# Kernel tuning notes

Measured on AMD Instinct MI355X. Metric: run time of the kernel, lower is better.

Reference implementation:

```python
import math
import jax, jax.numpy as jnp
import numpy as np

B, S, G, D = 16, 256, 2048, 512
H = 8
DK = D // H  # per-head key dim
E = 8        # num experts
TOPK = 2


def setup_inputs() -> dict:
    key = jax.random.key(0)
    ks = jax.random.split(key, 12)
    init = lambda k, shape, fan_in: jax.random.uniform(k, shape, jnp.float32, -1.0, 1.0) / np.sqrt(fan_in)
    return {
        'query': jax.random.normal(ks[0], (B, S, D), jnp.float32),
        'key': jax.random.normal(ks[1], (B, G, D), jnp.float32),
        'value': jax.random.normal(ks[2], (B, G, D), jnp.float32),  # unused by module (MHA uses h=key)
        'logit_key': jax.random.normal(ks[3], (B, G, D), jnp.float32),
        'attn_mask': jnp.zeros((B, G), dtype=bool),
        'Wq': init(ks[4], (H, D, DK), D),
        'Wk': init(ks[5], (H, D, DK), D),
        'Wv': init(ks[6], (H, D, DK), D),
        'Wo': init(ks[7], (H, DK, D), DK),
        'w_gate': jnp.zeros((D, E), jnp.float32) + init(ks[8], (D, E), D) * 0.0 + init(ks[9], (D, E), D),
        'expert_w': init(ks[10], (E, D, D), D),
    }


def _mha_glimpse(query, h, attn_mask, Wq, Wk, Wv, Wo):
    # Kool-style MHA: K and V both derived from h
    Q = jnp.einsum('bsd,hdk->bhsk', query, Wq)
    K = jnp.einsum('bgd,hdk->bhgk', h, Wk)
    V = jnp.einsum('bgd,hdk->bhgk', h, Wv)
    scores = jnp.einsum('bhsk,bhgk->bhsg', Q, K) / math.sqrt(DK)
    # 2D mask (B,G) expanded over heads and steps; True = masked out
    mask = attn_mask[:, None, None, :]
    scores = jnp.where(mask, jnp.float32(-1e9), scores)
    attn = jax.nn.softmax(scores, axis=-1)
    heads = jnp.einsum('bhsg,bhgk->bhsk', attn, V)
    return jnp.einsum('bhsk,hkd->bsd', heads, Wo)


def _moe(x, w_gate, expert_w):
    # x: (N, D). Noisy top-k gating, eval mode (no noise): clean logits -> top-k -> softmax over top-k.
    logits = x @ w_gate                                  # (N, E)
    top_vals, top_idx = jax.lax.top_k(logits, TOPK)      # (N, k)
    top_gates = jax.nn.softmax(top_vals, axis=-1)        # (N, k)
    gates = jnp.sum(jax.nn.one_hot(top_idx, E, dtype=x.dtype) * top_gates[..., None], axis=1)  # (N, E)
    expert_out = jnp.einsum('nd,edo->neo', x, expert_w)  # dense combine: same math as dispatch/scatter
    return jnp.einsum('ne,neo->no', gates, expert_out)


def reference(query, key, value, logit_key, attn_mask, Wq, Wk, Wv, Wo, w_gate, expert_w):
    glimpse = _mha_glimpse(query, key, attn_mask, Wq, Wk, Wv, Wo)  # (B, S, D)
    gm = _moe(glimpse.reshape(B * S, D), w_gate, expert_w).reshape(B, S, D)
    logits = jnp.einsum('bsd,bgd->bsg', gm, logit_key) / math.sqrt(D)
    return logits
```

## Files before the change

kernel.cpp:

```cpp
#include <hip/hip_runtime.h>

#define B_  16
#define S_  256
#define G_  2048
#define D_  512
#define H_  8
#define DK_ 64
#define E_  8

typedef _Float16 half8  __attribute__((ext_vector_type(8)));
typedef _Float16 half4v __attribute__((ext_vector_type(4)));
typedef float    floatx4 __attribute__((ext_vector_type(4)));

#define GLDS(g, l) __builtin_amdgcn_global_load_lds( \
    (const __attribute__((address_space(1))) void*)(g), \
    (__attribute__((address_space(3))) void*)(l), 16, 0, 0)

__global__ void __launch_bounds__(256) split_f16(
    const float* __restrict__ src, _Float16* __restrict__ hi,
    _Float16* __restrict__ lo, int n4)
{
    int i = blockIdx.x * 256 + threadIdx.x;
    if (i >= n4) return;
    float4 v = ((const float4*)src)[i];
    half4v h, l;
    h[0] = (_Float16)v.x; h[1] = (_Float16)v.y;
    h[2] = (_Float16)v.z; h[3] = (_Float16)v.w;
    l[0] = (_Float16)(v.x - (float)h[0]); l[1] = (_Float16)(v.y - (float)h[1]);
    l[2] = (_Float16)(v.z - (float)h[2]); l[3] = (_Float16)(v.w - (float)h[3]);
    ((half4v*)hi)[i] = h;
    ((half4v*)lo)[i] = l;
}

__global__ void __launch_bounds__(256) transpose_split(
    const float* __restrict__ src, _Float16* __restrict__ hi,
    _Float16* __restrict__ lo, int R, int C)
{
    __shared__ float T[32][33];
    const int tid = threadIdx.x;
    const long zo = (long)blockIdx.z * R * C;
    const int r0 = blockIdx.y * 32, c0 = blockIdx.x * 32;
#pragma unroll
    for (int p = 0; p < 4; ++p) {
        int i = tid + p * 256;
        int lr = i >> 5, lc = i & 31;
        T[lr][lc] = src[zo + (long)(r0 + lr) * C + (c0 + lc)];
    }
    __syncthreads();
#pragma unroll
    for (int p = 0; p < 4; ++p) {
        int i = tid + p * 256;
        int orr = i >> 5, oc = i & 31;
        float v = T[oc][orr];
        _Float16 h = (_Float16)v;
        long o = zo + (long)(c0 + orr) * R + (r0 + oc);
        hi[o] = h;
        lo[o] = (_Float16)(v - (float)h);
    }
}

__global__ void __launch_bounds__(256) gemm_f16x3(
    const _Float16* __restrict__ Ah, const _Float16* __restrict__ Al,
    const _Float16* __restrict__ Bh, const _Float16* __restrict__ Bl,
    float* __restrict__ C, _Float16* __restrict__ Chi, _Float16* __restrict__ Clo,
    long ldc, long sAz, long sBz, long sCz, float alpha)
{
    __shared__ _Float16 Ash[128 * 32], Asl[128 * 32];
    __shared__ _Float16 Bsh[128 * 32], Bsl[128 * 32];
    const int tid = threadIdx.x;
    const int w = tid >> 6, lane = tid & 63;
    const int quad = lane >> 4, tn = lane & 15;
    const int wm = (w >> 1) * 64, wn = (w & 1) * 64;
    const int z = blockIdx.z;
    const long m0 = (long)blockIdx.y * 128;
    const long n0 = (long)blockIdx.x * 128;
    const _Float16* Agh = Ah + (z * sAz + m0) * 512;
    const _Float16* Agl = Al + (z * sAz + m0) * 512;
    const _Float16* Bgh = Bh + (z * sBz + n0) * 512;
    const _Float16* Bgl = Bl + (z * sBz + n0) * 512;
    const long glane = (long)(lane >> 2) * 512 + (lane & 3) * 8;

    floatx4 acc[4][4] = {};

    for (int k0 = 0; k0 < 512; k0 += 32) {
#pragma unroll
        for (int cc = 0; cc < 2; ++cc) {
            const int c = 2 * w + cc;
            const long go = (long)c * 16 * 512 + glane + k0;
            GLDS(Agh + go, Ash + c * 512);
            GLDS(Agl + go, Asl + c * 512);
            GLDS(Bgh + go, Bsh + c * 512);
            GLDS(Bgl + go, Bsl + c * 512);
        }
        asm volatile("s_waitcnt vmcnt(0)" ::: "memory");
        __syncthreads();

        half8 ah[4], al[4], bh[4], bl[4];
#pragma unroll
        for (int t = 0; t < 4; ++t) {
            ah[t] = *(const half8*)&Ash[(wm + t * 16 + tn) * 32 + quad * 8];
            al[t] = *(const half8*)&Asl[(wm + t * 16 + tn) * 32 + quad * 8];
            bh[t] = *(const half8*)&Bsh[(wn + t * 16 + tn) * 32 + quad * 8];
            bl[t] = *(const half8*)&Bsl[(wn + t * 16 + tn) * 32 + quad * 8];
        }
#pragma unroll
        for (int i = 0; i < 4; ++i)
#pragma unroll
            for (int j = 0; j < 4; ++j) {
                acc[i][j] = __builtin_amdgcn_mfma_f32_16x16x32_f16(ah[i], bh[j], acc[i][j], 0, 0, 0);
                acc[i][j] = __builtin_amdgcn_mfma_f32_16x16x32_f16(ah[i], bl[j], acc[i][j], 0, 0, 0);
                acc[i][j] = __builtin_amdgcn_mfma_f32_16x16x32_f16(al[i], bh[j], acc[i][j], 0, 0, 0);
            }
        __syncthreads();
    }

#pragma unroll
    for (int i = 0; i < 4; ++i) {
        const long row0 = m0 + wm + i * 16 + quad * 4;
#pragma unroll
        for (int r = 0; r < 4; ++r) {
            const long row = row0 + r;
#pragma unroll
            for (int j = 0; j < 4; ++j) {
                float v = acc[i][j][r] * alpha;
                const long o = (long)z * sCz + row * ldc + n0 + wn + j * 16 + tn;
                if (C) C[o] = v;
                if (Chi) {
                    _Float16 hh = (_Float16)v;
                    Chi[o] = hh;
                    Clo[o] = (_Float16)(v - (float)hh);
                }
            }
        }
    }
}

__global__ void __launch_bounds__(512) flash_mfma(
    const _Float16* __restrict__ qh, const _Float16* __restrict__ qlo,
    const _Float16* __restrict__ kh, const _Float16* __restrict__ kl,
    const _Float16* __restrict__ vh, const _Float16* __restrict__ vl,
    const unsigned char* __restrict__ mask,
    _Float16* __restrict__ hd_hi, _Float16* __restrict__ hd_lo)
{
    __shared__ half8 KH[512], KL[512], VH[512], VL[512];
    __shared__ float PLb[8 * 16 * 64];
    const int tid = threadIdx.x;
    const int wid = tid >> 6, lane = tid & 63;
    const int quad = lane >> 4, tn = lane & 15;
    const int h = blockIdx.y, b = blockIdx.z;
    const int s_base = blockIdx.x * 128 + wid * 16;
    const long tok0 = (long)b * S_ + s_base;
    float* Pw = PLb + wid * (16 * 64);
    const unsigned char* mb = mask + (long)b * G_;

    const long qoff = (tok0 + tn) * 512 + h * 64 + quad * 8;
    half8 qfh[2], qfl[2];
    qfh[0] = *(const half8*)(qh + qoff);
    qfh[1] = *(const half8*)(qh + qoff + 32);
    qfl[0] = *(const half8*)(qlo + qoff);
    qfl[1] = *(const half8*)(qlo + qoff + 32);

    const int sr = tid >> 3, sg = tid & 7;
    const int swz = sr * 8 + (sg ^ (sr & 7));
    const long kgbase = (long)b * G_ * 512 + h * 64 + sg * 8;
    const long vgbase = (long)(h * 64 + sr) * (B_ * G_) + (long)b * G_ + sg * 8;

    half8 pk0 = *(const half8*)(kh + kgbase + (long)sr * 512);
    half8 pk1 = *(const half8*)(kl + kgbase + (long)sr * 512);
    half8 pk2 = *(const half8*)(vh + vgbase);
    half8 pk3 = *(const half8*)(vl + vgbase);

    floatx4 accO[4] = {};
    float lsum[4] = {0.f, 0.f, 0.f, 0.f};

    for (int t = 0; t < 32; ++t) {
        KH[swz] = pk0; KL[swz] = pk1; VH[swz] = pk2; VL[swz] = pk3;
        __syncthreads();
        if (t < 31) {
            const int g1 = (t + 1) * 64;
            pk0 = *(const half8*)(kh + kgbase + (long)(g1 + sr) * 512);
            pk1 = *(const half8*)(kl + kgbase + (long)(g1 + sr) * 512);
            pk2 = *(const half8*)(vh + vgbase + g1);
            pk3 = *(const half8*)(vl + vgbase + g1);
        }
        const int g0 = t * 64;

        floatx4 accS[4] = {};
#pragma unroll
        for (int k0 = 0; k0 < 2; ++k0)
#pragma unroll
            for (int nj = 0; nj < 4; ++nj) {
                const int row = nj * 16 + tn;
                const int gi = row * 8 + ((k0 * 4 + quad) ^ (row & 7));
                half8 kbh = KH[gi], kbl = KL[gi];
                accS[nj] = __builtin_amdgcn_mfma_f32_16x16x32_f16(qfh[k0], kbh, accS[nj], 0, 0, 0);
                accS[nj] = __builtin_amdgcn_mfma_f32_16x16x32_f16(qfh[k0], kbl, accS[nj], 0, 0, 0);
                accS[nj] = __builtin_amdgcn_mfma_f32_16x16x32_f16(qfl[k0], kbh, accS[nj], 0, 0, 0);
            }

        float rs[4] = {0.f, 0.f, 0.f, 0.f};
#pragma unroll
        for (int nj = 0; nj < 4; ++nj) {
            const bool mk = mb[g0 + nj * 16 + tn] != 0;
#pragma unroll
            for (int rr = 0; rr < 4; ++rr) {
                float p = __builtin_exp2f(accS[nj][rr]);
                p = mk ? 0.0f : p;
                accS[nj][rr] = p;
                rs[rr] += p;
            }
        }
#pragma unroll
        for (int rr = 0; rr < 4; ++rr) {
            float v = rs[rr];
            v += __shfl_xor(v, 1); v += __shfl_xor(v, 2);
            v += __shfl_xor(v, 4); v += __shfl_xor(v, 8);
            lsum[rr] += v;
        }

#pragma unroll
        for (int nj = 0; nj < 4; ++nj)
#pragma unroll
            for (int rr = 0; rr < 4; ++rr) {
                const int srow = quad * 4 + rr;
                const int c = nj * 16 + tn;
                Pw[srow * 64 + ((((c >> 2) ^ srow) & 15) << 2) + (c & 3)] = accS[nj][rr];
            }
        asm volatile("s_waitcnt lgkmcnt(0)" ::: "memory");

#pragma unroll
        for (int k0 = 0; k0 < 2; ++k0) {
            const int ga = k0 * 8 + quad * 2;
            floatx4 p0 = *(floatx4*)&Pw[tn * 64 + (((ga ^ tn) & 15) << 2)];
            floatx4 p1 = *(floatx4*)&Pw[tn * 64 + ((((ga + 1) ^ tn) & 15) << 2)];
            half8 ph, pl;
#pragma unroll
            for (int e = 0; e < 8; ++e) {
                const float x = (e < 4) ? p0[e & 3] : p1[e & 3];
                const float hi = __uint_as_float(__float_as_uint(x) & 0xFFFFE000u);
                ph[e] = (_Float16)hi;
                pl[e] = (_Float16)(x - hi);
            }
#pragma unroll
            for (int nj = 0; nj < 4; ++nj) {
                const int row = nj * 16 + tn;
                const int gi = row * 8 + ((k0 * 4 + quad) ^ (row & 7));
                half8 vbh = VH[gi], vbl = VL[gi];
                accO[nj] = __builtin_amdgcn_mfma_f32_16x16x32_f16(ph, vbh, accO[nj], 0, 0, 0);
                accO[nj] = __builtin_amdgcn_mfma_f32_16x16x32_f16(ph, vbl, accO[nj], 0, 0, 0);
                accO[nj] = __builtin_amdgcn_mfma_f32_16x16x32_f16(pl, vbh, accO[nj], 0, 0, 0);
            }
        }
        __syncthreads();
    }

#pragma unroll
    for (int rr = 0; rr < 4; ++rr) {
        const float inv = 1.0f / lsum[rr];
        const long rbase = (tok0 + quad * 4 + rr) * 512 + h * 64 + tn;
#pragma unroll
        for (int nj = 0; nj < 4; ++nj) {
            const float o = accO[nj][rr] * inv;
            const _Float16 oh = (_Float16)o;
            hd_hi[rbase + nj * 16] = oh;
            hd_lo[rbase + nj * 16] = (_Float16)(o - (float)oh);
        }
    }
}

__global__ void __launch_bounds__(256) gate_topk(
    const _Float16* __restrict__ Xh, const _Float16* __restrict__ Xl,
    const float* __restrict__ wg, float* __restrict__ gates)
{
    __shared__ float W[512][8];
    __shared__ float Xs[256][37];
    const int tid = threadIdx.x;
    const int n0 = blockIdx.x * 256;
#pragma unroll
    for (int p = 0; p < 16; ++p) ((float*)W)[tid + p * 256] = wg[tid + p * 256];

    float acc[8] = {};
    for (int dc = 0; dc < 512; dc += 32) {
        __syncthreads();
#pragma unroll
        for (int p = 0; p < 8; ++p) {
            int f = tid + p * 256;
            int row = f >> 3, c4 = f & 7;
            long o = (long)(n0 + row) * 512 + dc + 4 * c4;
            half4v hv = *(const half4v*)(Xh + o);
            half4v lv = *(const half4v*)(Xl + o);
#pragma unroll
            for (int i = 0; i < 4; ++i) Xs[row][4 * c4 + i] = (float)hv[i] + (float)lv[i];
        }
        __syncthreads();
        for (int d2 = 0; d2 < 32; ++d2) {
            float xv = Xs[tid][d2];
#pragma unroll
            for (int e = 0; e < 8; ++e) acc[e] += xv * W[dc + d2][e];
        }
    }
    float v1 = -3.0e38f; int i1 = 0;
#pragma unroll
    for (int e = 0; e < 8; ++e) if (acc[e] > v1) { v1 = acc[e]; i1 = e; }
    float v2 = -3.0e38f; int i2 = -1;
#pragma unroll
    for (int e = 0; e < 8; ++e) if (e != i1 && acc[e] > v2) { v2 = acc[e]; i2 = e; }
    float t = __expf(v2 - v1);
    float g1 = 1.0f / (1.0f + t);
    float g2 = t / (1.0f + t);
#pragma unroll
    for (int e = 0; e < 8; ++e)
        gates[(long)(n0 + tid) * 8 + e] = (e == i1) ? g1 : ((e == i2) ? g2 : 0.0f);
}

__global__ void __launch_bounds__(256) combine_moe(
    const float* __restrict__ eo, const float* __restrict__ gates,
    _Float16* __restrict__ gh, _Float16* __restrict__ gl)
{
    const int idx = blockIdx.x * 256 + threadIdx.x;
    const int n = idx >> 7;
    const int c = (idx & 127) * 4;
    float g[8];
#pragma unroll
    for (int e = 0; e < 8; ++e) g[e] = gates[(long)n * 8 + e];
    float ax = 0.f, ay = 0.f, az = 0.f, aw = 0.f;
#pragma unroll
    for (int e = 0; e < 8; ++e) {
        if (g[e] != 0.0f) {
            float4 v = *(const float4*)(eo + (long)e * 2097152 + (long)n * 512 + c);
            ax += g[e] * v.x; ay += g[e] * v.y; az += g[e] * v.z; aw += g[e] * v.w;
        }
    }
    half4v h, l;
    h[0] = (_Float16)ax; h[1] = (_Float16)ay; h[2] = (_Float16)az; h[3] = (_Float16)aw;
    l[0] = (_Float16)(ax - (float)h[0]); l[1] = (_Float16)(ay - (float)h[1]);
    l[2] = (_Float16)(az - (float)h[2]); l[3] = (_Float16)(aw - (float)h[3]);
    *(half4v*)(gh + (long)n * 512 + c) = h;
    *(half4v*)(gl + (long)n * 512 + c) = l;
}

extern "C" void kernel_launch(void* const* d_in, const int* in_sizes, int n_in,
                              void* d_out, int out_size, void* d_ws, size_t ws_size,
                              hipStream_t stream) {
    const float* query     = (const float*)d_in[0];
    const float* key       = (const float*)d_in[1];
    const float* logit_key = (const float*)d_in[3];
    const unsigned char* mask = (const unsigned char*)d_in[4];
    const float* Wq = (const float*)d_in[5];
    const float* Wk = (const float*)d_in[6];
    const float* Wv = (const float*)d_in[7];
    const float* Wo = (const float*)d_in[8];
    const float* wg = (const float*)d_in[9];
    const float* Ew = (const float*)d_in[10];
    float* out = (float*)d_out;

    const size_t MBy = 1048576;
    char* W = (char*)d_ws;
    _Float16* q_hi  = (_Float16*)(W + 0 * MBy);
    _Float16* q_lo  = (_Float16*)(W + 4 * MBy);
    _Float16* kp_hi = (_Float16*)(W + 8 * MBy);
    _Float16* kp_lo = (_Float16*)(W + 40 * MBy);
    _Float16* vt_hi = (_Float16*)(W + 72 * MBy);
    _Float16* vt_lo = (_Float16*)(W + 104 * MBy);
    _Float16* kin_hi = (_Float16*)(W + 136 * MBy);
    _Float16* kin_lo = (_Float16*)(W + 168 * MBy);
    float*    eo    = (float*)(W + 136 * MBy);
    _Float16* lk_hi = (_Float16*)(W + 136 * MBy);
    _Float16* lk_lo = (_Float16*)(W + 168 * MBy);
    _Float16* wq_hi = (_Float16*)(W + 204 * MBy);
    _Float16* wq_lo = (_Float16*)(W + 204 * MBy + 524288);
    _Float16* wk_hi = (_Float16*)(W + 205 * MBy);
    _Float16* wk_lo = (_Float16*)(W + 205 * MBy + 524288);
    _Float16* wv_hi = (_Float16*)(W + 206 * MBy);
    _Float16* wv_lo = (_Float16*)(W + 206 * MBy + 524288);
    _Float16* wo_hi = (_Float16*)(W + 207 * MBy);
    _Float16* wo_lo = (_Float16*)(W + 207 * MBy + 524288);
    _Float16* ew_hi = (_Float16*)(W + 208 * MBy);
    _Float16* ew_lo = (_Float16*)(W + 212 * MBy);
    _Float16* qi_hi = (_Float16*)(W + 216 * MBy);
    _Float16* qi_lo = (_Float16*)(W + 220 * MBy);
    _Float16* hd_hi = (_Float16*)(W + 216 * MBy);
    _Float16* hd_lo = (_Float16*)(W + 220 * MBy);
    _Float16* gl_hi = (_Float16*)(W + 224 * MBy);
    _Float16* gl_lo = (_Float16*)(W + 228 * MBy);
    _Float16* gm_hi = (_Float16*)(W + 232 * MBy);
    _Float16* gm_lo = (_Float16*)(W + 236 * MBy);
    float*    gates = (float*)(W + 240 * MBy);

    dim3 blk(256);

    split_f16<<<dim3(16384), blk, 0, stream>>>(key, kin_hi, kin_lo, 4194304);
    split_f16<<<dim3(2048), blk, 0, stream>>>(query, qi_hi, qi_lo, 524288);
    transpose_split<<<dim3(2, 16, 8), blk, 0, stream>>>(Wq, wq_hi, wq_lo, 512, 64);
    transpose_split<<<dim3(2, 16, 8), blk, 0, stream>>>(Wk, wk_hi, wk_lo, 512, 64);
    transpose_split<<<dim3(2, 16, 8), blk, 0, stream>>>(Wv, wv_hi, wv_lo, 512, 64);
    transpose_split<<<dim3(16, 16, 1), blk, 0, stream>>>(Wo, wo_hi, wo_lo, 512, 512);
    transpose_split<<<dim3(16, 16, 8), blk, 0, stream>>>(Ew, ew_hi, ew_lo, 512, 512);

    gemm_f16x3<<<dim3(4, 32, 1), blk, 0, stream>>>(
        qi_hi, qi_lo, wq_hi, wq_lo, nullptr, q_hi, q_lo, 512, 0, 0, 0,
        0.1803368801111204f);
    gemm_f16x3<<<dim3(4, 256, 1), blk, 0, stream>>>(
        kin_hi, kin_lo, wk_hi, wk_lo, nullptr, kp_hi, kp_lo, 512, 0, 0, 0, 1.0f);
    gemm_f16x3<<<dim3(256, 4, 1), blk, 0, stream>>>(
        wv_hi, wv_lo, kin_hi, kin_lo, nullptr, vt_hi, vt_lo, (long)B_ * G_,
        0, 0, 0, 1.0f);

    flash_mfma<<<dim3(2, H_, B_), dim3(512), 0, stream>>>(
        q_hi, q_lo, kp_hi, kp_lo, vt_hi, vt_lo, mask, hd_hi, hd_lo);

    gemm_f16x3<<<dim3(4, 32, 1), blk, 0, stream>>>(
        hd_hi, hd_lo, wo_hi, wo_lo, nullptr, gl_hi, gl_lo, 512, 0, 0, 0, 1.0f);

    gate_topk<<<dim3(16), blk, 0, stream>>>(gl_hi, gl_lo, wg, gates);

    gemm_f16x3<<<dim3(4, 32, 8), blk, 0, stream>>>(
        gl_hi, gl_lo, ew_hi, ew_lo, eo, nullptr, nullptr, 512, 0, 512, 2097152, 1.0f);

    combine_moe<<<dim3(2048), blk, 0, stream>>>(eo, gates, gm_hi, gm_lo);

    split_f16<<<dim3(16384), blk, 0, stream>>>(logit_key, lk_hi, lk_lo, 4194304);

    gemm_f16x3<<<dim3(16, 2, 16), blk, 0, stream>>>(
        gm_hi, gm_lo, lk_hi, lk_lo, out, nullptr, nullptr, 2048,
        256, 2048, 524288, 0.04419417382415922f);
}
```

Measured before the change: 609.9 us.

## Split flash attention over key sequence halves and merge partials in a combine kernel

The flash attention grid is split into two halves along the key dimension G, doubling the block count from 256 to 512. Each block writes its unnormalized output accumulator and row sums in fp32 to a scratch region that reuses the freed key-input buffer. A new combine kernel adds the two partials, normalizes, and writes the hi/lo fp16 pair. The intent is to fill more CUs and hide latency in the attention stage, at the cost of an extra kernel launch and fp32 round trips through global memory.

New measurement: 627.1 us. +2.8%, slower.

```diff
diff --git a/kernel.cpp b/kernel.cpp
--- a/kernel.cpp
+++ b/kernel.cpp
@@ -140,7 +140,7 @@
     const _Float16* __restrict__ kh, const _Float16* __restrict__ kl,
     const _Float16* __restrict__ vh, const _Float16* __restrict__ vl,
     const unsigned char* __restrict__ mask,
-    _Float16* __restrict__ hd_hi, _Float16* __restrict__ hd_lo)
+    float* __restrict__ Opart, float* __restrict__ Lpart)
 {
     __shared__ half8 KH[512], KL[512], VH[512], VL[512];
     __shared__ float PLb[8 * 16 * 64];
@@ -148,7 +148,9 @@
     const int wid = tid >> 6, lane = tid & 63;
     const int quad = lane >> 4, tn = lane & 15;
     const int h = blockIdx.y, b = blockIdx.z;
-    const int s_base = blockIdx.x * 128 + wid * 16;
+    const int sblk = blockIdx.x & 1, gh = blockIdx.x >> 1;
+    const int gbase0 = gh * 1024;
+    const int s_base = sblk * 128 + wid * 16;
     const long tok0 = (long)b * S_ + s_base;
     float* Pw = PLb + wid * (16 * 64);
     const unsigned char* mb = mask + (long)b * G_;
@@ -165,25 +167,25 @@
     const long kgbase = (long)b * G_ * 512 + h * 64 + sg * 8;
     const long vgbase = (long)(h * 64 + sr) * (B_ * G_) + (long)b * G_ + sg * 8;
 
-    half8 pk0 = *(const half8*)(kh + kgbase + (long)sr * 512);
-    half8 pk1 = *(const half8*)(kl + kgbase + (long)sr * 512);
-    half8 pk2 = *(const half8*)(vh + vgbase);
-    half8 pk3 = *(const half8*)(vl + vgbase);
+    half8 pk0 = *(const half8*)(kh + kgbase + (long)(gbase0 + sr) * 512);
+    half8 pk1 = *(const half8*)(kl + kgbase + (long)(gbase0 + sr) * 512);
+    half8 pk2 = *(const half8*)(vh + vgbase + gbase0);
+    half8 pk3 = *(const half8*)(vl + vgbase + gbase0);
 
     floatx4 accO[4] = {};
     float lsum[4] = {0.f, 0.f, 0.f, 0.f};
 
-    for (int t = 0; t < 32; ++t) {
+    for (int t = 0; t < 16; ++t) {
         KH[swz] = pk0; KL[swz] = pk1; VH[swz] = pk2; VL[swz] = pk3;
         __syncthreads();
-        if (t < 31) {
-            const int g1 = (t + 1) * 64;
+        if (t < 15) {
+            const int g1 = gbase0 + (t + 1) * 64;
             pk0 = *(const half8*)(kh + kgbase + (long)(g1 + sr) * 512);
             pk1 = *(const half8*)(kl + kgbase + (long)(g1 + sr) * 512);
             pk2 = *(const half8*)(vh + vgbase + g1);
             pk3 = *(const half8*)(vl + vgbase + g1);
         }
-        const int g0 = t * 64;
+        const int g0 = gbase0 + t * 64;
 
         floatx4 accS[4] = {};
 #pragma unroll
@@ -254,18 +256,44 @@
         __syncthreads();
     }
 
+    float* Op = Opart + (long)gh * (4096L * 512);
 #pragma unroll
     for (int rr = 0; rr < 4; ++rr) {
-        const float inv = 1.0f / lsum[rr];
         const long rbase = (tok0 + quad * 4 + rr) * 512 + h * 64 + tn;
 #pragma unroll
-        for (int nj = 0; nj < 4; ++nj) {
-            const float o = accO[nj][rr] * inv;
-            const _Float16 oh = (_Float16)o;
-            hd_hi[rbase + nj * 16] = oh;
-            hd_lo[rbase + nj * 16] = (_Float16)(o - (float)oh);
-        }
-    }
+        for (int nj = 0; nj < 4; ++nj)
+            Op[rbase + nj * 16] = accO[nj][rr];
+    }
+    if (tn == 0) {
+#pragma unroll
+        for (int rr = 0; rr < 4; ++rr)
+            Lpart[(long)gh * 32768 + (tok0 + quad * 4 + rr) * 8 + h] = lsum[rr];
+    }
+}
+
+__global__ void __launch_bounds__(256) combine_flash(
+    const float* __restrict__ Op, const float* __restrict__ Lp,
+    _Float16* __restrict__ hd_hi, _Float16* __restrict__ hd_lo)
+{
+    const int idx = blockIdx.x * 256 + threadIdx.x;
+    const int n = idx >> 7;
+    const int c = (idx & 127) * 4;
+    const int h = c >> 6;
+    const float l = Lp[(long)n * 8 + h] + Lp[32768 + (long)n * 8 + h];
+    const float inv = 1.0f / l;
+    float4 a = *(const float4*)(Op + (long)n * 512 + c);
+    float4 d = *(const float4*)(Op + 2097152L + (long)n * 512 + c);
+    const float ox = (a.x + d.x) * inv;
+    const float oy = (a.y + d.y) * inv;
+    const float oz = (a.z + d.z) * inv;
+    const float ow = (a.w + d.w) * inv;
+    half4v hh, ll;
+    hh[0] = (_Float16)ox; hh[1] = (_Float16)oy;
+    hh[2] = (_Float16)oz; hh[3] = (_Float16)ow;
+    ll[0] = (_Float16)(ox - (float)hh[0]); ll[1] = (_Float16)(oy - (float)hh[1]);
+    ll[2] = (_Float16)(oz - (float)hh[2]); ll[3] = (_Float16)(ow - (float)hh[3]);
+    *(half4v*)(hd_hi + (long)n * 512 + c) = hh;
+    *(half4v*)(hd_lo + (long)n * 512 + c) = ll;
 }
 
 __global__ void __launch_bounds__(256) gate_topk(
@@ -364,6 +392,8 @@
     _Float16* vt_lo = (_Float16*)(W + 104 * MBy);
     _Float16* kin_hi = (_Float16*)(W + 136 * MBy);
     _Float16* kin_lo = (_Float16*)(W + 168 * MBy);
+    float*    Opart = (float*)(W + 136 * MBy);
+    float*    Lpart = (float*)(W + 153 * MBy);
     float*    eo    = (float*)(W + 136 * MBy);
     _Float16* lk_hi = (_Float16*)(W + 136 * MBy);
     _Float16* lk_lo = (_Float16*)(W + 168 * MBy);
@@ -406,8 +436,9 @@
         wv_hi, wv_lo, kin_hi, kin_lo, nullptr, vt_hi, vt_lo, (long)B_ * G_,
         0, 0, 0, 1.0f);
 
-    flash_mfma<<<dim3(2, H_, B_), dim3(512), 0, stream>>>(
-        q_hi, q_lo, kp_hi, kp_lo, vt_hi, vt_lo, mask, hd_hi, hd_lo);
+    flash_mfma<<<dim3(4, H_, B_), dim3(512), 0, stream>>>(
+        q_hi, q_lo, kp_hi, kp_lo, vt_hi, vt_lo, mask, Opart, Lpart);
+    combine_flash<<<dim3(2048), blk, 0, stream>>>(Opart, Lpart, hd_hi, hd_lo);
 
     gemm_f16x3<<<dim3(4, 32, 1), blk, 0, stream>>>(
         hd_hi, hd_lo, wo_hi, wo_lo, nullptr, gl_hi, gl_lo, 512, 0, 0, 0, 1.0f);
```
